# Performance work log

Measured on AMD Instinct MI355X. Metric: run time of the kernel, lower is better.

Reference implementation:

```python
import jax, jax.numpy as jnp
import numpy as np

E = 256; H = 8; HD = E // H
L_LEN = 300; A_LEN = 250
T = 768; B = 4
NEG = -1e9


def setup_inputs() -> dict:
    rng = jax.random.key(0)
    ks = jax.random.split(rng, 16)
    n = lambda k, s, sc=1.0: jax.random.normal(k, s, dtype=jnp.float32) * sc
    return {
        "query": n(ks[0], (T, B, E)),
        "key": n(ks[1], (T, B, E)),
        "value": n(ks[2], (T, B, E)),
        "in_proj_w": n(ks[3], (3 * E, E), 0.05),
        "in_proj_b": jnp.zeros((3 * E,), jnp.float32),
        "out_w": n(ks[4], (7, E, E), 0.05),
        "out_b": jnp.zeros((7, E), jnp.float32),
        "s_l_w": n(ks[5], (E, 4 * E), 0.05),
        "s_l_b": jnp.zeros((E,), jnp.float32),
        "s_a_w": n(ks[6], (E, 4 * E), 0.05),
        "s_a_b": jnp.zeros((E,), jnp.float32),
        "s_v_w": n(ks[7], (E, 4 * E), 0.05),
        "s_v_b": jnp.zeros((E,), jnp.float32),
        "final_w": n(ks[8], (E, E), 0.05),
        "final_b": jnp.zeros((E,), jnp.float32),
    }


def _forward(query, key, value, in_proj_w, in_proj_b, out_w, out_b,
             s_l_w, s_l_b, s_a_w, s_a_b, s_v_w, s_v_b, final_w, final_b):
    t, b, e = query.shape
    scaling = HD ** -0.5
    Wq, Wk, Wv = in_proj_w[:E], in_proj_w[E:2 * E], in_proj_w[2 * E:]
    bq, bk, bv = in_proj_b[:E], in_proj_b[E:2 * E], in_proj_b[2 * E:]
    q = (query @ Wq.T + bq) * scaling
    k = key @ Wk.T + bk
    v = value @ Wv.T + bv
    # (T, B, E) -> (B*H, T, HD)
    sh = lambda x: x.reshape(t, b * H, HD).transpose(1, 0, 2)
    q, k, v = sh(q), sh(k), sh(v)
    # shared QK^T, reused by all 7 masked branches
    scores = jnp.einsum('bth,bsh->bts', q, k)  # (B*H, T, T)
    idx = jnp.arange(t)
    seg = jnp.where(idx < L_LEN, 0, jnp.where(idx < L_LEN + A_LEN, 1, 2))

    def branch(i, mods):
        # m[j] = 1 iff position j belongs to one of the selected modalities
        m = sum((seg == s) for s in mods).astype(scores.dtype)  # (T,)
        # additive mask: in-set query attends only in-set keys; out-of-set
        # query rows get all -1e9 (uniform softmax, zeroed by row mask below)
        add = jnp.where((m[:, None] * m[None, :]) > 0, 0.0, NEG)
        w = jax.nn.softmax(scores + add, axis=-1) * m[None, :, None]
        o = jnp.einsum('bts,bsh->bth', w, v * m[None, :, None])
        o = o.transpose(1, 0, 2).reshape(t, b, e)
        return o @ out_w[i].T + out_b[i]

    attn_lav = branch(0, (0, 1, 2))
    attn_la = branch(1, (0, 1))
    attn_lv = branch(2, (0, 2))
    attn_av = branch(3, (1, 2))
    attn_l = branch(4, (0,))
    attn_a = branch(5, (1,))
    attn_v = branch(6, (2,))

    sl = jnp.concatenate([attn_lav, attn_la, attn_lv, attn_l], -1) @ s_l_w.T + s_l_b
    sa = jnp.concatenate([attn_lav, attn_la, attn_av, attn_a], -1) @ s_a_w.T + s_a_b
    sv = jnp.concatenate([attn_lav, attn_lv, attn_av, attn_v], -1) @ s_v_w.T + s_v_b
    return (sl + sa + sv) @ final_w.T + final_b


def reference(query, key, value, in_proj_w, in_proj_b, out_w, out_b,
              s_l_w, s_l_b, s_a_w, s_a_b, s_v_w, s_v_b, final_w, final_b):
    return _forward(query, key, value, in_proj_w, in_proj_b, out_w, out_b,
                    s_l_w, s_l_b, s_a_w, s_a_b, s_v_w, s_v_b, final_w, final_b)
```

## Files before the change

kernel.cpp:

```cpp
#include <hip/hip_runtime.h>
#include <hip/hip_bf16.h>

#define E 256
#define H 8
#define HD 32
#define T 768
#define B 4
#define BH 32

typedef __attribute__((ext_vector_type(8))) short bf16x8;
typedef __attribute__((ext_vector_type(4))) float f32x4;
typedef __attribute__((ext_vector_type(16))) float f32x16;

__device__ __forceinline__ float b2f(__hip_bfloat16 x) { return __bfloat162float(x); }

__device__ __forceinline__ unsigned short f2bf_u(float x) {
    __hip_bfloat16 h = __float2bfloat16(x);
    return *(unsigned short*)&h;
}
__device__ __forceinline__ float bfu2f(unsigned short u) {
    return __uint_as_float(((unsigned int)u) << 16);
}

__device__ __forceinline__ int detect_f32(const void* query) {
    const unsigned short* q = (const unsigned short*)query;
    int lane = threadIdx.x & 63;
    int bad = 0;
    #pragma unroll
    for (int i = 0; i < 4; ++i) {
        float v = bfu2f(q[lane + i * 64]);
        bad |= (!(v == v) || fabsf(v) > 1e4f) ? 1 : 0;
    }
    return __any(bad) ? 1 : 0;
}

__device__ __forceinline__ void f8_split(const float* v, bf16x8& h, bf16x8& l) {
    #pragma unroll
    for (int e = 0; e < 8; ++e) {
        unsigned short hu = f2bf_u(v[e]);
        h[e] = (short)hu;
        l[e] = (short)f2bf_u(v[e] - bfu2f(hu));
    }
}

#define MFMA3(ACC, AH, AL, BH_, BL_)                                         \
    ACC = __builtin_amdgcn_mfma_f32_16x16x32_bf16(AH, BH_, ACC, 0, 0, 0);    \
    ACC = __builtin_amdgcn_mfma_f32_16x16x32_bf16(AH, BL_, ACC, 0, 0, 0);    \
    ACC = __builtin_amdgcn_mfma_f32_16x16x32_bf16(AL, BH_, ACC, 0, 0, 0);

#define MFMA3W(ACC, AH, AL, BH_, BL_)                                        \
    ACC = __builtin_amdgcn_mfma_f32_32x32x16_bf16(AH, BH_, ACC, 0, 0, 0);    \
    ACC = __builtin_amdgcn_mfma_f32_32x32x16_bf16(AH, BL_, ACC, 0, 0, 0);    \
    ACC = __builtin_amdgcn_mfma_f32_32x32x16_bf16(AL, BH_, ACC, 0, 0, 0);

__device__ __forceinline__ bf16x8 mk8(int a, int b, int c, int d) {
    union { int i[4]; bf16x8 v; } u;
    u.i[0] = a; u.i[1] = b; u.i[2] = c; u.i[3] = d;
    return u.v;
}

__device__ __forceinline__ float ldu(const void* p, size_t i, int f32) {
    if (f32) return ((const float*)p)[i];
    return b2f(((const __hip_bfloat16*)p)[i]);
}

__device__ __forceinline__ float gsum_load(int i, int r2, int r,
                                           const void* sl, const void* sa,
                                           const void* sv, int f32)
{
    size_t base = (size_t)r2 * 1024;
    switch (i) {
        case 0: return ldu(sl, base + r, f32) + ldu(sa, base + r, f32) + ldu(sv, base + r, f32);
        case 1: return ldu(sl, base + 256 + r, f32) + ldu(sa, base + 256 + r, f32);
        case 2: return ldu(sl, base + 512 + r, f32) + ldu(sv, base + 256 + r, f32);
        case 3: return ldu(sa, base + 512 + r, f32) + ldu(sv, base + 512 + r, f32);
        case 4: return ldu(sl, base + 768 + r, f32);
        case 5: return ldu(sa, base + 768 + r, f32);
        default: return ldu(sv, base + 768 + r, f32);
    }
}

__global__ __launch_bounds__(256) void stage1_kernel(
    const void* query, const void* w,
    const void* sl, const void* sa, const void* sv, const void* outw,
    const void* outb, const void* slb, const void* sab, const void* svb,
    unsigned short* __restrict__ WFh, unsigned short* __restrict__ WFl,
    unsigned short* __restrict__ GFh, unsigned short* __restrict__ GFl,
    unsigned short* __restrict__ OWFh, unsigned short* __restrict__ OWFl,
    float* __restrict__ c0)
{
    __shared__ float red[256];
    int f32 = detect_f32(query);
    if (blockIdx.x < 544) {
        int item = blockIdx.x * 256 + threadIdx.x;
        if (item < 24576) {
            int gc = item >> 5, kg = item & 31;
            float v[8];
            if (f32) {
                const float4* p = (const float4*)((const float*)w +
                                   (size_t)gc * 256 + kg * 8);
                *(float4*)&v[0] = p[0];
                *(float4*)&v[4] = p[1];
            } else {
                #pragma unroll
                for (int j = 0; j < 8; ++j)
                    v[j] = ldu(w, (size_t)gc * 256 + kg * 8 + j, 0);
            }
            bf16x8 h, l;
            f8_split(v, h, l);
            int sec = gc >> 8, c = gc & 255;
            int cb = c >> 4, kb = kg >> 2;
            int lane = (c & 15) | ((kg & 3) << 4);
            size_t idx = (((size_t)(sec * 16 + cb) * 8 + kb) * 64 + lane) * 8;
            *(bf16x8*)&WFh[idx] = h;
            *(bf16x8*)&WFl[idx] = l;
        } else if (item < 81920) {
            int rem = item - 24576;
            int i = rem >> 13;
            int rest = rem & 8191;
            int r2 = rest >> 5, kg = rest & 31;
            float v[8];
            #pragma unroll
            for (int j = 0; j < 8; ++j)
                v[j] = gsum_load(i, r2, kg * 8 + j, sl, sa, sv, f32);
            bf16x8 h, l;
            f8_split(v, h, l);
            int rb = r2 >> 4, kb = kg >> 2;
            int lane = (r2 & 15) | ((kg & 3) << 4);
            size_t idx = (((size_t)(i * 16 + rb) * 8 + kb) * 64 + lane) * 8;
            *(bf16x8*)&GFh[idx] = h;
            *(bf16x8*)&GFl[idx] = l;
        } else if (item < 139264) {
            int rem = item - 81920;
            int i = rem >> 13;
            int rest = rem & 8191;
            int kg = rest >> 8, c = rest & 255;
            float v[8];
            #pragma unroll
            for (int j = 0; j < 8; ++j)
                v[j] = ldu(outw, (size_t)i * 65536 + (kg * 8 + j) * 256 + c, f32);
            bf16x8 h, l;
            f8_split(v, h, l);
            int cb = c >> 4, kb = kg >> 2;
            int lane = (c & 15) | ((kg & 3) << 4);
            size_t idx = (((size_t)(i * 16 + cb) * 8 + kb) * 64 + lane) * 8;
            *(bf16x8*)&OWFh[idx] = h;
            *(bf16x8*)&OWFl[idx] = l;
        }
    } else {
        int r2 = blockIdx.x - 544, m = threadIdx.x;
        float acc = 0.f;
        #pragma unroll
        for (int i = 0; i < 7; ++i)
            acc += ldu(outb, i * 256 + m, f32) * gsum_load(i, r2, m, sl, sa, sv, f32);
        red[m] = acc;
        __syncthreads();
        for (int s = 128; s > 0; s >>= 1) {
            if (m < s) red[m] += red[m + s];
            __syncthreads();
        }
        if (m == 0)
            c0[r2] = red[0] + ldu(slb, r2, f32) + ldu(sab, r2, f32) + ldu(svb, r2, f32);
    }
}

__global__ __launch_bounds__(256) void stage2_kernel(
    const void* query, const void* key, const void* value,
    const unsigned short* __restrict__ WFh, const unsigned short* __restrict__ WFl,
    const void* bias,
    float* __restrict__ qws,
    unsigned short* __restrict__ KRh, unsigned short* __restrict__ KRl,
    unsigned short* __restrict__ VFh, unsigned short* __restrict__ VFl,
    const unsigned short* __restrict__ GFh, const unsigned short* __restrict__ GFl,
    const unsigned short* __restrict__ OWFh, const unsigned short* __restrict__ OWFl,
    float* __restrict__ Mtmp,
    const float* __restrict__ c0, const void* finalw, const void* finalb,
    float* __restrict__ d0)
{
    __shared__ float red[256];
    int bxx = blockIdx.x;
    if (bxx < 576) {
        int f32 = detect_f32(query);
        int sec = bxx / 192;
        int rb  = bxx % 192;
        const void* X = (sec == 0) ? query : (sec == 1) ? key : value;
        int w = threadIdx.x >> 6, lane = threadIdx.x & 63;
        int m = lane & 15, quad = lane >> 4;

        size_t aoff0 = (size_t)(rb * 16 + (lane & 15)) * 256 + quad * 8;

        f32x4 acc[4] = {};
        #pragma unroll
        for (int kb = 0; kb < 8; ++kb) {
            float av[8];
            size_t aoff = aoff0 + kb * 32;
            if (f32) {
                const float4* p = (const float4*)((const float*)X + aoff);
                *(float4*)&av[0] = p[0];
                *(float4*)&av[4] = p[1];
            } else {
                #pragma unroll
                for (int j = 0; j < 8; ++j)
                    av[j] = ldu(X, aoff + j, 0);
            }
            bf16x8 ah, al;
            f8_split(av, ah, al);
            #pragma unroll
            for (int c = 0; c < 4; ++c) {
                int cb = w * 4 + c;
                const unsigned short* Bh = WFh + (((size_t)(sec * 16 + cb) * 8 + kb) * 64 + lane) * 8;
                const unsigned short* Bl = WFl + (((size_t)(sec * 16 + cb) * 8 + kb) * 64 + lane) * 8;
                bf16x8 bh = *(const bf16x8*)Bh;
                bf16x8 bl = *(const bf16x8*)Bl;
                MFMA3(acc[c], ah, al, bh, bl)
            }
        }

        #pragma unroll
        for (int c = 0; c < 4; ++c) {
            int cb = w * 4 + c;
            int c_local = cb * 16 + m;
            float bv = ldu(bias, sec * 256 + c_local, f32);
            int h = c_local >> 5, hd = c_local & 31;

            if (sec == 0) {
                #pragma unroll
                for (int rr = 0; rr < 4; ++rr) {
                    int row = rb * 16 + quad * 4 + rr;
                    int t = row >> 2, b = row & 3;
                    float val = (acc[c][rr] + bv) * 0.17677669529663687f;
                    qws[((size_t)((b * H + h) * T + t)) * HD + hd] = val;
                }
            } else if (sec == 1) {
                #pragma unroll
                for (int rr = 0; rr < 4; ++rr) {
                    int row = rb * 16 + quad * 4 + rr;
                    int s = row >> 2, b = row & 3;
                    int bh_ = b * 8 + h;
                    float val = acc[c][rr] + bv;
                    unsigned short hu = f2bf_u(val);
                    unsigned short lu = f2bf_u(val - bfu2f(hu));
                    size_t bi = ((size_t)bh_ * 768 + s) * 32 + hd;
                    KRh[bi] = hu;
                    KRl[bi] = lu;
                }
            } else {
                #pragma unroll
                for (int rr = 0; rr < 4; ++rr) {
                    int row = rb * 16 + quad * 4 + rr;
                    int s = row >> 2, b = row & 3;
                    int bh_ = b * 8 + h;
                    float val = acc[c][rr] + bv;
                    unsigned short hu = f2bf_u(val);
                    unsigned short lu = f2bf_u(val - bfu2f(hu));
                    int s16 = s >> 4, hp = (s >> 3) & 1, j = s & 7;
                    size_t bi = (((size_t)bh_ * 48 + s16) * 64 + hp * 32 + hd) * 8 + j;
                    VFh[bi] = hu;
                    VFl[bi] = lu;
                }
            }
        }
    } else if (bxx < 1024) {
        int idx = bxx - 576;
        int cgrp = idx & 3;
        int rb   = (idx >> 2) & 15;
        int i    = idx >> 6;
        int w = threadIdx.x >> 6, lane = threadIdx.x & 63;
        int m = lane & 15, quad = lane >> 4;
        int cb = cgrp * 4 + w;

        const unsigned short* Ah = GFh + (((size_t)(i * 16 + rb) * 8) * 64 + lane) * 8;
        const unsigned short* Al = GFl + (((size_t)(i * 16 + rb) * 8) * 64 + lane) * 8;
        const unsigned short* Bh = OWFh + (((size_t)(i * 16 + cb) * 8) * 64 + lane) * 8;
        const unsigned short* Bl = OWFl + (((size_t)(i * 16 + cb) * 8) * 64 + lane) * 8;

        f32x4 acc = {};
        #pragma unroll
        for (int kb = 0; kb < 8; ++kb) {
            size_t off = (size_t)kb * 512;
            bf16x8 ah = *(const bf16x8*)(Ah + off);
            bf16x8 al = *(const bf16x8*)(Al + off);
            bf16x8 bh = *(const bf16x8*)(Bh + off);
            bf16x8 bl = *(const bf16x8*)(Bl + off);
            MFMA3(acc, ah, al, bh, bl)
        }
        #pragma unroll
        for (int rr = 0; rr < 4; ++rr) {
            int r2 = rb * 16 + quad * 4 + rr;
            Mtmp[(size_t)i * 65536 + r2 * 256 + cb * 16 + m] = acc[rr];
        }
    } else {
        int f32 = detect_f32(query);
        int e = bxx - 1024, r = threadIdx.x;
        red[r] = c0[r] * ldu(finalw, (size_t)e * 256 + r, f32);
        __syncthreads();
        for (int s = 128; s > 0; s >>= 1) {
            if (r < s) red[r] += red[r + s];
            __syncthreads();
        }
        if (r == 0)
            d0[e] = red[0] + ldu(finalb, e, f32);
    }
}

__global__ __launch_bounds__(256, 2) void stage3_kernel(
    const float* __restrict__ qws,
    const unsigned short* __restrict__ KRh, const unsigned short* __restrict__ KRl,
    const unsigned short* __restrict__ VFh, const unsigned short* __restrict__ VFl,
    unsigned short* __restrict__ Ohi, unsigned short* __restrict__ Olo,
    const float* __restrict__ Mtmp, const void* finalw, const void* query,
    unsigned short* __restrict__ DThi, unsigned short* __restrict__ DTlo)
{
    __shared__ __align__(16) float SMEM[7104];
    int tid = threadIdx.x;

    if (blockIdx.x < 768) {
        float (*AC2)[3][32][36] = (float(*)[3][32][36])&SMEM[0];
        float (*SS2)[3][32]     = (float(*)[3][32])&SMEM[6912];
        int bid = blockIdx.x;
        int xcd = bid & 7, rr_ = bid >> 3;
        int j_ = rr_ / 24, tile = rr_ % 24;
        int bh = j_ * 8 + xcd;
        int t0 = tile * 32;
        int w = tid >> 6, lane = tid & 63;
        int ln = lane & 31, h = lane >> 5;

        bf16x8 qbh[2], qbl[2];
        {
            const float* qr = qws + ((size_t)bh * T + t0 + ln) * HD + h * 8;
            #pragma unroll
            for (int c = 0; c < 2; ++c) {
                float qv[8];
                *(float4*)&qv[0] = *(const float4*)(qr + c * 16);
                *(float4*)&qv[4] = *(const float4*)(qr + c * 16 + 4);
                f8_split(qv, qbh[c], qbl[c]);
            }
        }

        f32x16 accA = {}, accB = {};
        float ssA = 0.f, ssB = 0.f;

        for (int q = 0; q < 3; ++q) {
            int ch = w * 3 + q;
            int sbase = ch * 64;
            int route = (ch == 5) ? 1 : (ch == 4 || ch == 8) ? 2 : 0;
            int bnd = (ch == 4) ? 300 : 550;
            bool c12 = (ch == 4);

            bf16x8 kf0h[2], kf0l[2], kf1h[2], kf1l[2], vh[4], vl[4];
            #pragma unroll
            for (int st = 0; st < 2; ++st) {
                size_t krow = ((size_t)bh * 768 + sbase + st * 32 + ln) * 32 + h * 8;
                kf0h[st] = *(const bf16x8*)(KRh + krow);
                kf0l[st] = *(const bf16x8*)(KRl + krow);
                kf1h[st] = *(const bf16x8*)(KRh + krow + 16);
                kf1l[st] = *(const bf16x8*)(KRl + krow + 16);
            }
            #pragma unroll
            for (int ks = 0; ks < 4; ++ks) {
                size_t vidx = (((size_t)bh * 48 + ch * 4 + ks) * 64 + lane) * 8;
                vh[ks] = *(const bf16x8*)(VFh + vidx);
                vl[ks] = *(const bf16x8*)(VFl + vidx);
            }

            #pragma unroll
            for (int st = 0; st < 2; ++st) {
                f32x16 d = {};
                MFMA3W(d, kf0h[st], kf0l[st], qbh[0], qbl[0])
                MFMA3W(d, kf1h[st], kf1l[st], qbh[1], qbl[1])

                int PH[8], PL[8];
                #pragma unroll
                for (int p = 0; p < 8; ++p) {
                    float e0 = __expf(d[2 * p]);
                    float e1 = __expf(d[2 * p + 1]);
                    if (route == 2) {
                        int r0 = 2 * p;
                        int s0 = sbase + st * 32 + (r0 & 3) + 8 * (r0 >> 2) + 4 * h;
                        if (s0 < bnd) ssA += e0; else ssB += e0;
                        if (s0 + 1 < bnd) ssA += e1; else ssB += e1;
                    } else if (route == 1) { ssB += e0 + e1; }
                    else { ssA += e0 + e1; }
                    unsigned b0 = __float_as_uint(e0), b1 = __float_as_uint(e1);
                    float l0 = e0 - __uint_as_float(b0 & 0xffff0000u);
                    float l1 = e1 - __uint_as_float(b1 & 0xffff0000u);
                    PH[p] = (int)((b0 >> 16) | (b1 & 0xffff0000u));
                    PL[p] = (int)((__float_as_uint(l0) >> 16) |
                                  (__float_as_uint(l1) & 0xffff0000u));
                }

                #pragma unroll
                for (int ksl = 0; ksl < 2; ++ksl) {
                    int ks = st * 2 + ksl;
                    int cc = 4 * ksl;
                    bf16x8 vbh = vh[ks];
                    bf16x8 vbl = vl[ks];

                    int sh0 = __shfl_xor(PH[cc+0], 32);
                    int sh1 = __shfl_xor(PH[cc+1], 32);
                    int sh2 = __shfl_xor(PH[cc+2], 32);
                    int sh3 = __shfl_xor(PH[cc+3], 32);
                    int sl0 = __shfl_xor(PL[cc+0], 32);
                    int sl1 = __shfl_xor(PL[cc+1], 32);
                    int sl2 = __shfl_xor(PL[cc+2], 32);
                    int sl3 = __shfl_xor(PL[cc+3], 32);
                    int FH0 = h ? sh2 : PH[cc+0];
                    int FH1 = h ? sh3 : PH[cc+1];
                    int FH2 = h ? PH[cc+2] : sh0;
                    int FH3 = h ? PH[cc+3] : sh1;
                    int FL0 = h ? sl2 : PL[cc+0];
                    int FL1 = h ? sl3 : PL[cc+1];
                    int FL2 = h ? PL[cc+2] : sl0;
                    int FL3 = h ? PL[cc+3] : sl1;
                    bf16x8 feh = mk8(FH0, FH1, FH2, FH3);
                    bf16x8 fel = mk8(FL0, FL1, FL2, FL3);

                    if (route == 0)      { MFMA3W(accA, feh, fel, vbh, vbl) }
                    else if (route == 1) { MFMA3W(accB, feh, fel, vbh, vbl) }
                    else {
                        if (ks < 2)       { MFMA3W(accA, feh, fel, vbh, vbl) }
                        else if (ks == 3) { MFMA3W(accB, feh, fel, vbh, vbl) }
                        else {
                            int a0 = h ? (c12 ? FH0 : 0) : FH0;
                            int a1 = h ? (c12 ? FH1 : 0) : FH1;
                            int a2 = h ? 0 : FH2;
                            int a3 = h ? 0 : (c12 ? FH3 : 0);
                            int b0 = h ? (c12 ? 0 : FH0) : 0;
                            int b1 = h ? (c12 ? 0 : FH1) : 0;
                            int b2 = h ? FH2 : 0;
                            int b3 = h ? FH3 : (c12 ? 0 : FH3);
                            int la0 = h ? (c12 ? FL0 : 0) : FL0;
                            int la1 = h ? (c12 ? FL1 : 0) : FL1;
                            int la2 = h ? 0 : FL2;
                            int la3 = h ? 0 : (c12 ? FL3 : 0);
                            int lb0 = h ? (c12 ? 0 : FL0) : 0;
                            int lb1 = h ? (c12 ? 0 : FL1) : 0;
                            int lb2 = h ? FL2 : 0;
                            int lb3 = h ? FL3 : (c12 ? 0 : FL3);
                            bf16x8 fha = mk8(a0, a1, a2, a3), fla = mk8(la0, la1, la2, la3);
                            bf16x8 fhb = mk8(b0, b1, b2, b3), flb = mk8(lb0, lb1, lb2, lb3);
                            MFMA3W(accA, fha, fla, vbh, vbl)
                            MFMA3W(accB, fhb, flb, vbh, vbl)
                        }
                    }
                }
            }
        }

        ssA += __shfl_xor(ssA, 32);
        ssB += __shfl_xor(ssB, 32);

        int bsel = w & 1;
        f32x16 zz = {};
        f32x16 o0 = (w <= 1) ? accA : zz;
        f32x16 o1 = (w == 1) ? accB : (w == 2) ? accA : zz;
        f32x16 o2 = (w == 2) ? accB : (w == 3) ? accA : zz;
        float s0 = (w <= 1) ? ssA : 0.f;
        float s1 = (w == 1) ? ssB : (w == 2) ? ssA : 0.f;
        float s2 = (w == 2) ? ssB : (w == 3) ? ssA : 0.f;

        if (w < 2) {
            #pragma unroll
            for (int r = 0; r < 16; ++r) {
                int t = (r & 3) + 8 * (r >> 2) + 4 * h;
                AC2[bsel][0][t][ln] = o0[r];
                AC2[bsel][1][t][ln] = o1[r];
                AC2[bsel][2][t][ln] = o2[r];
            }
            if (h == 0) {
                SS2[bsel][0][ln] = s0;
                SS2[bsel][1][ln] = s1;
                SS2[bsel][2][ln] = s2;
            }
        }
        __syncthreads();
        if (w >= 2) {
            #pragma unroll
            for (int r = 0; r < 16; ++r) {
                int t = (r & 3) + 8 * (r >> 2) + 4 * h;
                AC2[bsel][1][t][ln] += o1[r];
                AC2[bsel][2][t][ln] += o2[r];
            }
            if (h == 0) {
                SS2[bsel][1][ln] += s1;
                SS2[bsel][2][ln] += s2;
            }
        }
        __syncthreads();

        int tt = tid >> 3, q4 = tid & 7;
        float Pv[3][4], S[3];
        #pragma unroll
        for (int sg = 0; sg < 3; ++sg) {
            const float4 a = *(const float4*)&AC2[0][sg][tt][q4 * 4];
            const float4 b = *(const float4*)&AC2[1][sg][tt][q4 * 4];
            Pv[sg][0] = a.x + b.x; Pv[sg][1] = a.y + b.y;
            Pv[sg][2] = a.z + b.z; Pv[sg][3] = a.w + b.w;
            S[sg] = SS2[0][sg][tt] + SS2[1][sg][tt];
        }

        int t_glob = t0 + tt;
        int g = (t_glob < 300) ? 0 : (t_glob < 550 ? 1 : 2);
        int b_ = bh >> 3, h_ = bh & 7;
        int row = b_ * T + t_glob;
        int lslot = (row & 15) + ((q4 >> 1) << 4);
        int j0 = (q4 & 1) * 4;
        size_t fbase = (((size_t)(row >> 4) * 56 + h_) * 64 + lslot) * 8 + j0;
        const int masks[7] = {7, 3, 5, 6, 1, 2, 4};
        #pragma unroll
        for (int i = 0; i < 7; ++i) {
            int mm = masks[i];
            float n0 = 0.f, n1 = 0.f, n2 = 0.f, n3 = 0.f, den = 0.f;
            if (mm & 1) { n0 += Pv[0][0]; n1 += Pv[0][1]; n2 += Pv[0][2]; n3 += Pv[0][3]; den += S[0]; }
            if (mm & 2) { n0 += Pv[1][0]; n1 += Pv[1][1]; n2 += Pv[1][2]; n3 += Pv[1][3]; den += S[1]; }
            if (mm & 4) { n0 += Pv[2][0]; n1 += Pv[2][1]; n2 += Pv[2][2]; n3 += Pv[2][3]; den += S[2]; }
            float r = 1.f / den;
            int live = (mm >> g) & 1;
            float o[4];
            o[0] = live ? n0 * r : 0.f;
            o[1] = live ? n1 * r : 0.f;
            o[2] = live ? n2 * r : 0.f;
            o[3] = live ? n3 * r : 0.f;
            ushort4 hi4, lo4;
            unsigned short* hp = (unsigned short*)&hi4;
            unsigned short* lp = (unsigned short*)&lo4;
            #pragma unroll
            for (int jq = 0; jq < 4; ++jq) {
                unsigned short hu = f2bf_u(o[jq]);
                hp[jq] = hu;
                lp[jq] = f2bf_u(o[jq] - bfu2f(hu));
            }
            size_t addr = fbase + (size_t)i * (8 * 64 * 8);
            *(ushort4*)&Ohi[addr] = hi4;
            *(ushort4*)&Olo[addr] = lo4;
        }
    } else {
        float (*AsT)[34] = (float(*)[34])&SMEM[0];
        float (*Bs)[34]  = (float(*)[34])&SMEM[1088];
        int f32 = detect_f32(query);
        int idx = blockIdx.x - 768;
        int bx = idx & 7;
        int by = (idx >> 3) & 7;
        int i  = idx >> 6;
        int tx = tid & 15, ty = tid >> 4;
        int colbase = bx * 32, rowbase = by * 32;
        float acc[2][2] = {};

        for (int kb = 0; kb < 8; ++kb) {
            __syncthreads();
            #pragma unroll
            for (int l = 0; l < 4; ++l) {
                int idx2 = l * 256 + tid;
                int c = idx2 & 31, kk = idx2 >> 5;
                AsT[kk][c] = Mtmp[(size_t)i * 65536 + (kb * 32 + kk) * 256 + rowbase + c];
                int k2 = idx2 & 31, n = idx2 >> 5;
                Bs[k2][n] = ldu(finalw, (size_t)(colbase + n) * 256 + kb * 32 + k2, f32);
            }
            __syncthreads();
            #pragma unroll 8
            for (int kk = 0; kk < 32; ++kk) {
                const float2 av = *(const float2*)&AsT[kk][ty * 2];
                const float2 bv = *(const float2*)&Bs[kk][tx * 2];
                acc[0][0] += av.x * bv.x; acc[0][1] += av.x * bv.y;
                acc[1][0] += av.y * bv.x; acc[1][1] += av.y * bv.y;
            }
        }
        #pragma unroll
        for (int u = 0; u < 2; ++u)
            #pragma unroll
            for (int v = 0; v < 2; ++v) {
                int c = rowbase + ty * 2 + u, e = colbase + tx * 2 + v;
                float a = acc[u][v];
                unsigned short hu = f2bf_u(a);
                size_t fidx = (((size_t)(e >> 4) * 56 + i * 8 + (c >> 5)) * 64
                               + (e & 15) + (((c >> 3) & 3) << 4)) * 8 + (c & 7);
                DThi[fidx] = hu;
                DTlo[fidx] = f2bf_u(a - bfu2f(hu));
            }
    }
}

__global__ __launch_bounds__(256) void final_gemm_mfma_kernel(
    const unsigned short* __restrict__ Ohi, const unsigned short* __restrict__ Olo,
    const unsigned short* __restrict__ DThi, const unsigned short* __restrict__ DTlo,
    const float* __restrict__ d0, const void* query,
    void* __restrict__ outv)
{
    int f32 = detect_f32(query);
    int bid = blockIdx.x;
    int xcd = bid & 7, rr_ = bid >> 3;
    int slot = rr_ >> 2, bx = rr_ & 3;
    int by = slot * 8 + xcd;
    int w  = threadIdx.x >> 6;
    int lane = threadIdx.x & 63;
    int m = lane & 15, quad = lane >> 4;
    int R0 = by * 16, C0 = bx * 64 + w * 16;

    int b_out = R0 / 768;
    int tfirst = R0 - b_out * 768;
    int g0 = (tfirst < 300) ? 0 : (tfirst < 550 ? 1 : 2);
    int g1 = (tfirst + 15 < 300) ? 0 : (tfirst + 15 < 550 ? 1 : 2);
    int activeset = (1 << g0) | (1 << g1);
    const int masks[7] = {7, 3, 5, 6, 1, 2, 4};

    const unsigned short* Abase_h = Ohi + (size_t)by * 56 * 512 + lane * 8;
    const unsigned short* Abase_l = Olo + (size_t)by * 56 * 512 + lane * 8;
    const unsigned short* Bbase_h = DThi + (size_t)(bx * 4 + w) * 56 * 512 + lane * 8;
    const unsigned short* Bbase_l = DTlo + (size_t)(bx * 4 + w) * 56 * 512 + lane * 8;

    f32x4 acc = {};
    for (int i = 0; i < 7; ++i) {
        if (!(masks[i] & activeset)) continue;
        #pragma unroll
        for (int kb = 0; kb < 8; ++kb) {
            size_t off = (size_t)(i * 8 + kb) * 512;
            bf16x8 ah = *(const bf16x8*)(Abase_h + off);
            bf16x8 al = *(const bf16x8*)(Abase_l + off);
            bf16x8 bh = *(const bf16x8*)(Bbase_h + off);
            bf16x8 bl = *(const bf16x8*)(Bbase_l + off);
            acc = __builtin_amdgcn_mfma_f32_16x16x32_bf16(ah, bh, acc, 0, 0, 0);
            acc = __builtin_amdgcn_mfma_f32_16x16x32_bf16(ah, bl, acc, 0, 0, 0);
            acc = __builtin_amdgcn_mfma_f32_16x16x32_bf16(al, bh, acc, 0, 0, 0);
        }
    }
    float dv = d0[C0 + m];
    #pragma unroll
    for (int r = 0; r < 4; ++r) {
        int t = tfirst + quad * 4 + r;
        int col = C0 + m;
        float val = acc[r] + dv;
        size_t orow = (size_t)t * B + b_out;
        if (f32) ((float*)outv)[orow * 256 + col] = val;
        else ((__hip_bfloat16*)outv)[orow * 256 + col] = __float2bfloat16(val);
    }
}

extern "C" void kernel_launch(void* const* d_in, const int* in_sizes, int n_in,
                              void* d_out, int out_size, void* d_ws, size_t ws_size,
                              hipStream_t stream) {
    const void* query     = d_in[0];
    const void* key       = d_in[1];
    const void* value     = d_in[2];
    const void* in_proj_w = d_in[3];
    const void* in_proj_b = d_in[4];
    const void* out_w     = d_in[5];
    const void* out_b     = d_in[6];
    const void* s_l_w     = d_in[7];
    const void* s_l_b     = d_in[8];
    const void* s_a_w     = d_in[9];
    const void* s_a_b     = d_in[10];
    const void* s_v_w     = d_in[11];
    const void* s_v_b     = d_in[12];
    const void* final_w   = d_in[13];
    const void* final_b   = d_in[14];

    float* ws     = (float*)d_ws;
    float* qws    = ws;
    unsigned short* KRh = (unsigned short*)(ws + 786432);
    unsigned short* KRl = KRh + 786432;
    unsigned short* VFh = (unsigned short*)(ws + 1572864);
    unsigned short* VFl = VFh + 786432;
    unsigned short* Ohi = (unsigned short*)(ws + 2359296);
    unsigned short* Olo = (unsigned short*)(ws + 5111808);
    unsigned short* WFh = (unsigned short*)(ws + 2359296);
    unsigned short* WFl = WFh + 196608;
    unsigned short* GFh = (unsigned short*)(ws + 4915200);
    unsigned short* GFl = GFh + 458752;
    unsigned short* OWFh = GFl + 458752;
    unsigned short* OWFl = OWFh + 458752;
    float* Mtmp   = ws + 7864320;
    unsigned short* DThi = (unsigned short*)(ws + 8323072);
    unsigned short* DTlo = (unsigned short*)(ws + 8552448);
    float* d0     = ws + 8781824;
    float* c0     = ws + 8782336;

    stage1_kernel<<<800, 256, 0, stream>>>(query, in_proj_w,
                                           s_l_w, s_a_w, s_v_w, out_w,
                                           out_b, s_l_b, s_a_b, s_v_b,
                                           WFh, WFl,
                                           GFh, GFl, OWFh, OWFl, c0);
    stage2_kernel<<<1280, 256, 0, stream>>>(query, key, value,
                                            WFh, WFl, in_proj_b, qws,
                                            KRh, KRl, VFh, VFl,
                                            GFh, GFl, OWFh, OWFl, Mtmp,
                                            c0, final_w, final_b, d0);
    stage3_kernel<<<1216, 256, 0, stream>>>(qws, KRh, KRl, VFh, VFl,
                                            Ohi, Olo,
                                            Mtmp, final_w, query,
                                            DThi, DTlo);
    final_gemm_mfma_kernel<<<768, 256, 0, stream>>>(Ohi, Olo, DThi, DTlo,
                                                    d0, query, d_out);
}
```

Before: 160.4 us.

## Reassociate folded weight products to move final_w GEMM off the attention stage

The weight-folding chain is reordered. final_w × Gsum_i is now computed first in stage1 with MFMA into Qbuf, and stage2 multiplies that by out_w_i and writes the DT fragments directly. This removes the GF split buffers and the scalar FP32 LDS-tiled GEMM that used to run as extra blocks inside the attention kernel (stage3), so stage3 only does attention with 768 blocks. The cost is heavier stage1 blocks that gather gsum values element-wise, and a changed rounding order for the folded weights.

```diff
diff --git a/kernel.cpp b/kernel.cpp
--- a/kernel.cpp
+++ b/kernel.cpp
@@ -84,15 +84,16 @@
     const void* query, const void* w,
     const void* sl, const void* sa, const void* sv, const void* outw,
     const void* outb, const void* slb, const void* sab, const void* svb,
+    const void* finalw,
     unsigned short* __restrict__ WFh, unsigned short* __restrict__ WFl,
-    unsigned short* __restrict__ GFh, unsigned short* __restrict__ GFl,
     unsigned short* __restrict__ OWFh, unsigned short* __restrict__ OWFl,
-    float* __restrict__ c0)
+    float* __restrict__ Qbuf, float* __restrict__ c0)
 {
     __shared__ float red[256];
     int f32 = detect_f32(query);
-    if (blockIdx.x < 544) {
-        int item = blockIdx.x * 256 + threadIdx.x;
+    int bid = blockIdx.x;
+    if (bid < 320) {
+        int item = bid * 256 + threadIdx.x;
         if (item < 24576) {
             int gc = item >> 5, kg = item & 31;
             float v[8];
@@ -118,22 +119,6 @@
             int rem = item - 24576;
             int i = rem >> 13;
             int rest = rem & 8191;
-            int r2 = rest >> 5, kg = rest & 31;
-            float v[8];
-            #pragma unroll
-            for (int j = 0; j < 8; ++j)
-                v[j] = gsum_load(i, r2, kg * 8 + j, sl, sa, sv, f32);
-            bf16x8 h, l;
-            f8_split(v, h, l);
-            int rb = r2 >> 4, kb = kg >> 2;
-            int lane = (r2 & 15) | ((kg & 3) << 4);
-            size_t idx = (((size_t)(i * 16 + rb) * 8 + kb) * 64 + lane) * 8;
-            *(bf16x8*)&GFh[idx] = h;
-            *(bf16x8*)&GFl[idx] = l;
-        } else if (item < 139264) {
-            int rem = item - 81920;
-            int i = rem >> 13;
-            int rest = rem & 8191;
             int kg = rest >> 8, c = rest & 255;
             float v[8];
             #pragma unroll
@@ -147,8 +132,47 @@
             *(bf16x8*)&OWFh[idx] = h;
             *(bf16x8*)&OWFl[idx] = l;
         }
+    } else if (bid < 768) {
+        int unit = bid - 320;
+        int kgrp = unit & 3;
+        int eb   = (unit >> 2) & 15;
+        int i    = unit >> 6;
+        int w_ = threadIdx.x >> 6, lane = threadIdx.x & 63;
+        int m = lane & 15, quad = lane >> 4;
+        int kblk = kgrp * 4 + w_;
+
+        f32x4 acc = {};
+        #pragma unroll
+        for (int rb2 = 0; rb2 < 8; ++rb2) {
+            float av[8];
+            size_t fo = (size_t)(eb * 16 + m) * 256 + rb2 * 32 + quad * 8;
+            if (f32) {
+                const float4* p = (const float4*)((const float*)finalw + fo);
+                *(float4*)&av[0] = p[0];
+                *(float4*)&av[4] = p[1];
+            } else {
+                #pragma unroll
+                for (int j = 0; j < 8; ++j)
+                    av[j] = ldu(finalw, fo + j, 0);
+            }
+            bf16x8 ah, al;
+            f8_split(av, ah, al);
+            float bv[8];
+            #pragma unroll
+            for (int j = 0; j < 8; ++j)
+                bv[j] = gsum_load(i, rb2 * 32 + quad * 8 + j, kblk * 16 + m,
+                                  sl, sa, sv, f32);
+            bf16x8 bh, bl;
+            f8_split(bv, bh, bl);
+            MFMA3(acc, ah, al, bh, bl)
+        }
+        #pragma unroll
+        for (int rr = 0; rr < 4; ++rr) {
+            int e_ = eb * 16 + quad * 4 + rr;
+            Qbuf[(size_t)i * 65536 + e_ * 256 + kblk * 16 + m] = acc[rr];
+        }
     } else {
-        int r2 = blockIdx.x - 544, m = threadIdx.x;
+        int r2 = bid - 768, m = threadIdx.x;
         float acc = 0.f;
         #pragma unroll
         for (int i = 0; i < 7; ++i)
@@ -171,9 +195,9 @@
     float* __restrict__ qws,
     unsigned short* __restrict__ KRh, unsigned short* __restrict__ KRl,
     unsigned short* __restrict__ VFh, unsigned short* __restrict__ VFl,
-    const unsigned short* __restrict__ GFh, const unsigned short* __restrict__ GFl,
     const unsigned short* __restrict__ OWFh, const unsigned short* __restrict__ OWFl,
-    float* __restrict__ Mtmp,
+    const float* __restrict__ Qbuf,
+    unsigned short* __restrict__ DThi, unsigned short* __restrict__ DTlo,
     const float* __restrict__ c0, const void* finalw, const void* finalb,
     float* __restrict__ d0)
 {
@@ -261,33 +285,40 @@
             }
         }
     } else if (bxx < 1024) {
-        int idx = bxx - 576;
-        int cgrp = idx & 3;
-        int rb   = (idx >> 2) & 15;
-        int i    = idx >> 6;
+        int unit = bxx - 576;
+        int cgrp = unit & 3;
+        int eb   = (unit >> 2) & 15;
+        int i    = unit >> 6;
         int w = threadIdx.x >> 6, lane = threadIdx.x & 63;
         int m = lane & 15, quad = lane >> 4;
         int cb = cgrp * 4 + w;
 
-        const unsigned short* Ah = GFh + (((size_t)(i * 16 + rb) * 8) * 64 + lane) * 8;
-        const unsigned short* Al = GFl + (((size_t)(i * 16 + rb) * 8) * 64 + lane) * 8;
-        const unsigned short* Bh = OWFh + (((size_t)(i * 16 + cb) * 8) * 64 + lane) * 8;
-        const unsigned short* Bl = OWFl + (((size_t)(i * 16 + cb) * 8) * 64 + lane) * 8;
-
         f32x4 acc = {};
         #pragma unroll
         for (int kb = 0; kb < 8; ++kb) {
-            size_t off = (size_t)kb * 512;
-            bf16x8 ah = *(const bf16x8*)(Ah + off);
-            bf16x8 al = *(const bf16x8*)(Al + off);
-            bf16x8 bh = *(const bf16x8*)(Bh + off);
-            bf16x8 bl = *(const bf16x8*)(Bl + off);
+            float av[8];
+            const float* qp = Qbuf + (size_t)i * 65536 +
+                              (size_t)(eb * 16 + m) * 256 + kb * 32 + quad * 8;
+            *(float4*)&av[0] = *(const float4*)qp;
+            *(float4*)&av[4] = *(const float4*)(qp + 4);
+            bf16x8 ah, al;
+            f8_split(av, ah, al);
+            const unsigned short* Bh = OWFh + (((size_t)(i * 16 + cb) * 8 + kb) * 64 + lane) * 8;
+            const unsigned short* Bl = OWFl + (((size_t)(i * 16 + cb) * 8 + kb) * 64 + lane) * 8;
+            bf16x8 bh = *(const bf16x8*)Bh;
+            bf16x8 bl = *(const bf16x8*)Bl;
             MFMA3(acc, ah, al, bh, bl)
         }
         #pragma unroll
         for (int rr = 0; rr < 4; ++rr) {
-            int r2 = rb * 16 + quad * 4 + rr;
-            Mtmp[(size_t)i * 65536 + r2 * 256 + cb * 16 + m] = acc[rr];
+            int e_ = eb * 16 + quad * 4 + rr;
+            int c_ = cb * 16 + m;
+            float a = acc[rr];
+            unsigned short hu = f2bf_u(a);
+            size_t fidx = (((size_t)(e_ >> 4) * 56 + i * 8 + (c_ >> 5)) * 64
+                           + (e_ & 15) + (((c_ >> 3) & 3) << 4)) * 8 + (c_ & 7);
+            DThi[fidx] = hu;
+            DTlo[fidx] = f2bf_u(a - bfu2f(hu));
         }
     } else {
         int f32 = detect_f32(query);
@@ -307,276 +338,231 @@
     const float* __restrict__ qws,
     const unsigned short* __restrict__ KRh, const unsigned short* __restrict__ KRl,
     const unsigned short* __restrict__ VFh, const unsigned short* __restrict__ VFl,
-    unsigned short* __restrict__ Ohi, unsigned short* __restrict__ Olo,
-    const float* __restrict__ Mtmp, const void* finalw, const void* query,
-    unsigned short* __restrict__ DThi, unsigned short* __restrict__ DTlo)
+    unsigned short* __restrict__ Ohi, unsigned short* __restrict__ Olo)
 {
     __shared__ __align__(16) float SMEM[7104];
     int tid = threadIdx.x;
 
-    if (blockIdx.x < 768) {
-        float (*AC2)[3][32][36] = (float(*)[3][32][36])&SMEM[0];
-        float (*SS2)[3][32]     = (float(*)[3][32])&SMEM[6912];
-        int bid = blockIdx.x;
-        int xcd = bid & 7, rr_ = bid >> 3;
-        int j_ = rr_ / 24, tile = rr_ % 24;
-        int bh = j_ * 8 + xcd;
-        int t0 = tile * 32;
-        int w = tid >> 6, lane = tid & 63;
-        int ln = lane & 31, h = lane >> 5;
-
-        bf16x8 qbh[2], qbl[2];
-        {
-            const float* qr = qws + ((size_t)bh * T + t0 + ln) * HD + h * 8;
+    float (*AC2)[3][32][36] = (float(*)[3][32][36])&SMEM[0];
+    float (*SS2)[3][32]     = (float(*)[3][32])&SMEM[6912];
+    int bid = blockIdx.x;
+    int xcd = bid & 7, rr_ = bid >> 3;
+    int j_ = rr_ / 24, tile = rr_ % 24;
+    int bh = j_ * 8 + xcd;
+    int t0 = tile * 32;
+    int w = tid >> 6, lane = tid & 63;
+    int ln = lane & 31, h = lane >> 5;
+
+    bf16x8 qbh[2], qbl[2];
+    {
+        const float* qr = qws + ((size_t)bh * T + t0 + ln) * HD + h * 8;
+        #pragma unroll
+        for (int c = 0; c < 2; ++c) {
+            float qv[8];
+            *(float4*)&qv[0] = *(const float4*)(qr + c * 16);
+            *(float4*)&qv[4] = *(const float4*)(qr + c * 16 + 4);
+            f8_split(qv, qbh[c], qbl[c]);
+        }
+    }
+
+    f32x16 accA = {}, accB = {};
+    float ssA = 0.f, ssB = 0.f;
+
+    for (int q = 0; q < 3; ++q) {
+        int ch = w * 3 + q;
+        int sbase = ch * 64;
+        int route = (ch == 5) ? 1 : (ch == 4 || ch == 8) ? 2 : 0;
+        int bnd = (ch == 4) ? 300 : 550;
+        bool c12 = (ch == 4);
+
+        bf16x8 kf0h[2], kf0l[2], kf1h[2], kf1l[2], vh[4], vl[4];
+        #pragma unroll
+        for (int st = 0; st < 2; ++st) {
+            size_t krow = ((size_t)bh * 768 + sbase + st * 32 + ln) * 32 + h * 8;
+            kf0h[st] = *(const bf16x8*)(KRh + krow);
+            kf0l[st] = *(const bf16x8*)(KRl + krow);
+            kf1h[st] = *(const bf16x8*)(KRh + krow + 16);
+            kf1l[st] = *(const bf16x8*)(KRl + krow + 16);
+        }
+        #pragma unroll
+        for (int ks = 0; ks < 4; ++ks) {
+            size_t vidx = (((size_t)bh * 48 + ch * 4 + ks) * 64 + lane) * 8;
+            vh[ks] = *(const bf16x8*)(VFh + vidx);
+            vl[ks] = *(const bf16x8*)(VFl + vidx);
+        }
+
+        #pragma unroll
+        for (int st = 0; st < 2; ++st) {
+            f32x16 d = {};
+            MFMA3W(d, kf0h[st], kf0l[st], qbh[0], qbl[0])
+            MFMA3W(d, kf1h[st], kf1l[st], qbh[1], qbl[1])
+
+            int PH[8], PL[8];
             #pragma unroll
-            for (int c = 0; c < 2; ++c) {
-                float qv[8];
-                *(float4*)&qv[0] = *(const float4*)(qr + c * 16);
-                *(float4*)&qv[4] = *(const float4*)(qr + c * 16 + 4);
-                f8_split(qv, qbh[c], qbl[c]);
+            for (int p = 0; p < 8; ++p) {
+                float e0 = __expf(d[2 * p]);
+                float e1 = __expf(d[2 * p + 1]);
+                if (route == 2) {
+                    int r0 = 2 * p;
+                    int s0 = sbase + st * 32 + (r0 & 3) + 8 * (r0 >> 2) + 4 * h;
+                    if (s0 < bnd) ssA += e0; else ssB += e0;
+                    if (s0 + 1 < bnd) ssA += e1; else ssB += e1;
+                } else if (route == 1) { ssB += e0 + e1; }
+                else { ssA += e0 + e1; }
+                unsigned b0 = __float_as_uint(e0), b1 = __float_as_uint(e1);
+                float l0 = e0 - __uint_as_float(b0 & 0xffff0000u);
+                float l1 = e1 - __uint_as_float(b1 & 0xffff0000u);
+                PH[p] = (int)((b0 >> 16) | (b1 & 0xffff0000u));
+                PL[p] = (int)((__float_as_uint(l0) >> 16) |
+                              (__float_as_uint(l1) & 0xffff0000u));
             }
-        }
-
-        f32x16 accA = {}, accB = {};
-        float ssA = 0.f, ssB = 0.f;
-
-        for (int q = 0; q < 3; ++q) {
-            int ch = w * 3 + q;
-            int sbase = ch * 64;
-            int route = (ch == 5) ? 1 : (ch == 4 || ch == 8) ? 2 : 0;
-            int bnd = (ch == 4) ? 300 : 550;
-            bool c12 = (ch == 4);
-
-            bf16x8 kf0h[2], kf0l[2], kf1h[2], kf1l[2], vh[4], vl[4];
+
             #pragma unroll
-            for (int st = 0; st < 2; ++st) {
-                size_t krow = ((size_t)bh * 768 + sbase + st * 32 + ln) * 32 + h * 8;
-                kf0h[st] = *(const bf16x8*)(KRh + krow);
-                kf0l[st] = *(const bf16x8*)(KRl + krow);
-                kf1h[st] = *(const bf16x8*)(KRh + krow + 16);
-                kf1l[st] = *(const bf16x8*)(KRl + krow + 16);
-            }
-            #pragma unroll
-            for (int ks = 0; ks < 4; ++ks) {
-                size_t vidx = (((size_t)bh * 48 + ch * 4 + ks) * 64 + lane) * 8;
-                vh[ks] = *(const bf16x8*)(VFh + vidx);
-                vl[ks] = *(const bf16x8*)(VFl + vidx);
-            }
-
-            #pragma unroll
-            for (int st = 0; st < 2; ++st) {
-                f32x16 d = {};
-                MFMA3W(d, kf0h[st], kf0l[st], qbh[0], qbl[0])
-                MFMA3W(d, kf1h[st], kf1l[st], qbh[1], qbl[1])
-
-                int PH[8], PL[8];
-                #pragma unroll
-                for (int p = 0; p < 8; ++p) {
-                    float e0 = __expf(d[2 * p]);
-                    float e1 = __expf(d[2 * p + 1]);
-                    if (route == 2) {
-                        int r0 = 2 * p;
-                        int s0 = sbase + st * 32 + (r0 & 3) + 8 * (r0 >> 2) + 4 * h;
-                        if (s0 < bnd) ssA += e0; else ssB += e0;
-                        if (s0 + 1 < bnd) ssA += e1; else ssB += e1;
-                    } else if (route == 1) { ssB += e0 + e1; }
-                    else { ssA += e0 + e1; }
-                    unsigned b0 = __float_as_uint(e0), b1 = __float_as_uint(e1);
-                    float l0 = e0 - __uint_as_float(b0 & 0xffff0000u);
-                    float l1 = e1 - __uint_as_float(b1 & 0xffff0000u);
-                    PH[p] = (int)((b0 >> 16) | (b1 & 0xffff0000u));
-                    PL[p] = (int)((__float_as_uint(l0) >> 16) |
-                                  (__float_as_uint(l1) & 0xffff0000u));
-                }
-
-                #pragma unroll
-                for (int ksl = 0; ksl < 2; ++ksl) {
-                    int ks = st * 2 + ksl;
-                    int cc = 4 * ksl;
-                    bf16x8 vbh = vh[ks];
-                    bf16x8 vbl = vl[ks];
-
-                    int sh0 = __shfl_xor(PH[cc+0], 32);
-                    int sh1 = __shfl_xor(PH[cc+1], 32);
-                    int sh2 = __shfl_xor(PH[cc+2], 32);
-                    int sh3 = __shfl_xor(PH[cc+3], 32);
-                    int sl0 = __shfl_xor(PL[cc+0], 32);
-                    int sl1 = __shfl_xor(PL[cc+1], 32);
-                    int sl2 = __shfl_xor(PL[cc+2], 32);
-                    int sl3 = __shfl_xor(PL[cc+3], 32);
-                    int FH0 = h ? sh2 : PH[cc+0];
-                    int FH1 = h ? sh3 : PH[cc+1];
-                    int FH2 = h ? PH[cc+2] : sh0;
-                    int FH3 = h ? PH[cc+3] : sh1;
-                    int FL0 = h ? sl2 : PL[cc+0];
-                    int FL1 = h ? sl3 : PL[cc+1];
-                    int FL2 = h ? PL[cc+2] : sl0;
-                    int FL3 = h ? PL[cc+3] : sl1;
-                    bf16x8 feh = mk8(FH0, FH1, FH2, FH3);
-                    bf16x8 fel = mk8(FL0, FL1, FL2, FL3);
-
-                    if (route == 0)      { MFMA3W(accA, feh, fel, vbh, vbl) }
-                    else if (route == 1) { MFMA3W(accB, feh, fel, vbh, vbl) }
+            for (int ksl = 0; ksl < 2; ++ksl) {
+                int ks = st * 2 + ksl;
+                int cc = 4 * ksl;
+                bf16x8 vbh = vh[ks];
+                bf16x8 vbl = vl[ks];
+
+                int sh0 = __shfl_xor(PH[cc+0], 32);
+                int sh1 = __shfl_xor(PH[cc+1], 32);
+                int sh2 = __shfl_xor(PH[cc+2], 32);
+                int sh3 = __shfl_xor(PH[cc+3], 32);
+                int sl0 = __shfl_xor(PL[cc+0], 32);
+                int sl1 = __shfl_xor(PL[cc+1], 32);
+                int sl2 = __shfl_xor(PL[cc+2], 32);
+                int sl3 = __shfl_xor(PL[cc+3], 32);
+                int FH0 = h ? sh2 : PH[cc+0];
+                int FH1 = h ? sh3 : PH[cc+1];
+                int FH2 = h ? PH[cc+2] : sh0;
+                int FH3 = h ? PH[cc+3] : sh1;
+                int FL0 = h ? sl2 : PL[cc+0];
+                int FL1 = h ? sl3 : PL[cc+1];
+                int FL2 = h ? PL[cc+2] : sl0;
+                int FL3 = h ? PL[cc+3] : sl1;
+                bf16x8 feh = mk8(FH0, FH1, FH2, FH3);
+                bf16x8 fel = mk8(FL0, FL1, FL2, FL3);
+
+                if (route == 0)      { MFMA3W(accA, feh, fel, vbh, vbl) }
+                else if (route == 1) { MFMA3W(accB, feh, fel, vbh, vbl) }
+                else {
+                    if (ks < 2)       { MFMA3W(accA, feh, fel, vbh, vbl) }
+                    else if (ks == 3) { MFMA3W(accB, feh, fel, vbh, vbl) }
                     else {
-                        if (ks < 2)       { MFMA3W(accA, feh, fel, vbh, vbl) }
-                        else if (ks == 3) { MFMA3W(accB, feh, fel, vbh, vbl) }
-                        else {
-                            int a0 = h ? (c12 ? FH0 : 0) : FH0;
-                            int a1 = h ? (c12 ? FH1 : 0) : FH1;
-                            int a2 = h ? 0 : FH2;
-                            int a3 = h ? 0 : (c12 ? FH3 : 0);
-                            int b0 = h ? (c12 ? 0 : FH0) : 0;
-                            int b1 = h ? (c12 ? 0 : FH1) : 0;
-                            int b2 = h ? FH2 : 0;
-                            int b3 = h ? FH3 : (c12 ? 0 : FH3);
-                            int la0 = h ? (c12 ? FL0 : 0) : FL0;
-                            int la1 = h ? (c12 ? FL1 : 0) : FL1;
-                            int la2 = h ? 0 : FL2;
-                            int la3 = h ? 0 : (c12 ? FL3 : 0);
-                            int lb0 = h ? (c12 ? 0 : FL0) : 0;
-                            int lb1 = h ? (c12 ? 0 : FL1) : 0;
-                            int lb2 = h ? FL2 : 0;
-                            int lb3 = h ? FL3 : (c12 ? 0 : FL3);
-                            bf16x8 fha = mk8(a0, a1, a2, a3), fla = mk8(la0, la1, la2, la3);
-                            bf16x8 fhb = mk8(b0, b1, b2, b3), flb = mk8(lb0, lb1, lb2, lb3);
-                            MFMA3W(accA, fha, fla, vbh, vbl)
-                            MFMA3W(accB, fhb, flb, vbh, vbl)
-                        }
+                        int a0 = h ? (c12 ? FH0 : 0) : FH0;
+                        int a1 = h ? (c12 ? FH1 : 0) : FH1;
+                        int a2 = h ? 0 : FH2;
+                        int a3 = h ? 0 : (c12 ? FH3 : 0);
+                        int b0 = h ? (c12 ? 0 : FH0) : 0;
+                        int b1 = h ? (c12 ? 0 : FH1) : 0;
+                        int b2 = h ? FH2 : 0;
+                        int b3 = h ? FH3 : (c12 ? 0 : FH3);
+                        int la0 = h ? (c12 ? FL0 : 0) : FL0;
+                        int la1 = h ? (c12 ? FL1 : 0) : FL1;
+                        int la2 = h ? 0 : FL2;
+                        int la3 = h ? 0 : (c12 ? FL3 : 0);
+                        int lb0 = h ? (c12 ? 0 : FL0) : 0;
+                        int lb1 = h ? (c12 ? 0 : FL1) : 0;
+                        int lb2 = h ? FL2 : 0;
+                        int lb3 = h ? FL3 : (c12 ? 0 : FL3);
+                        bf16x8 fha = mk8(a0, a1, a2, a3), fla = mk8(la0, la1, la2, la3);
+                        bf16x8 fhb = mk8(b0, b1, b2, b3), flb = mk8(lb0, lb1, lb2, lb3);
+                        MFMA3W(accA, fha, fla, vbh, vbl)
+                        MFMA3W(accB, fhb, flb, vbh, vbl)
                     }
                 }
             }
         }
-
-        ssA += __shfl_xor(ssA, 32);
-        ssB += __shfl_xor(ssB, 32);
-
-        int bsel = w & 1;
-        f32x16 zz = {};
-        f32x16 o0 = (w <= 1) ? accA : zz;
-        f32x16 o1 = (w == 1) ? accB : (w == 2) ? accA : zz;
-        f32x16 o2 = (w == 2) ? accB : (w == 3) ? accA : zz;
-        float s0 = (w <= 1) ? ssA : 0.f;
-        float s1 = (w == 1) ? ssB : (w == 2) ? ssA : 0.f;
-        float s2 = (w == 2) ? ssB : (w == 3) ? ssA : 0.f;
-
-        if (w < 2) {
-            #pragma unroll
-            for (int r = 0; r < 16; ++r) {
-                int t = (r & 3) + 8 * (r >> 2) + 4 * h;
-                AC2[bsel][0][t][ln] = o0[r];
-                AC2[bsel][1][t][ln] = o1[r];
-                AC2[bsel][2][t][ln] = o2[r];
-            }
-            if (h == 0) {
-                SS2[bsel][0][ln] = s0;
-                SS2[bsel][1][ln] = s1;
-                SS2[bsel][2][ln] = s2;
-            }
-        }
-        __syncthreads();
-        if (w >= 2) {
-            #pragma unroll
-            for (int r = 0; r < 16; ++r) {
-                int t = (r & 3) + 8 * (r >> 2) + 4 * h;
-                AC2[bsel][1][t][ln] += o1[r];
-                AC2[bsel][2][t][ln] += o2[r];
-            }
-            if (h == 0) {
-                SS2[bsel][1][ln] += s1;
-                SS2[bsel][2][ln] += s2;
-            }
-        }
-        __syncthreads();
-
-        int tt = tid >> 3, q4 = tid & 7;
-        float Pv[3][4], S[3];
-        #pragma unroll
-        for (int sg = 0; sg < 3; ++sg) {
-            const float4 a = *(const float4*)&AC2[0][sg][tt][q4 * 4];
-            const float4 b = *(const float4*)&AC2[1][sg][tt][q4 * 4];
-            Pv[sg][0] = a.x + b.x; Pv[sg][1] = a.y + b.y;
-            Pv[sg][2] = a.z + b.z; Pv[sg][3] = a.w + b.w;
-            S[sg] = SS2[0][sg][tt] + SS2[1][sg][tt];
-        }
-
-        int t_glob = t0 + tt;
-        int g = (t_glob < 300) ? 0 : (t_glob < 550 ? 1 : 2);
-        int b_ = bh >> 3, h_ = bh & 7;
-        int row = b_ * T + t_glob;
-        int lslot = (row & 15) + ((q4 >> 1) << 4);
-        int j0 = (q4 & 1) * 4;
-        size_t fbase = (((size_t)(row >> 4) * 56 + h_) * 64 + lslot) * 8 + j0;
-        const int masks[7] = {7, 3, 5, 6, 1, 2, 4};
-        #pragma unroll
-        for (int i = 0; i < 7; ++i) {
-            int mm = masks[i];
-            float n0 = 0.f, n1 = 0.f, n2 = 0.f, n3 = 0.f, den = 0.f;
-            if (mm & 1) { n0 += Pv[0][0]; n1 += Pv[0][1]; n2 += Pv[0][2]; n3 += Pv[0][3]; den += S[0]; }
-            if (mm & 2) { n0 += Pv[1][0]; n1 += Pv[1][1]; n2 += Pv[1][2]; n3 += Pv[1][3]; den += S[1]; }
-            if (mm & 4) { n0 += Pv[2][0]; n1 += Pv[2][1]; n2 += Pv[2][2]; n3 += Pv[2][3]; den += S[2]; }
-            float r = 1.f / den;
-            int live = (mm >> g) & 1;
-            float o[4];
-            o[0] = live ? n0 * r : 0.f;
-            o[1] = live ? n1 * r : 0.f;
-            o[2] = live ? n2 * r : 0.f;
-            o[3] = live ? n3 * r : 0.f;
-            ushort4 hi4, lo4;
-            unsigned short* hp = (unsigned short*)&hi4;
-            unsigned short* lp = (unsigned short*)&lo4;
-            #pragma unroll
-            for (int jq = 0; jq < 4; ++jq) {
-                unsigned short hu = f2bf_u(o[jq]);
-                hp[jq] = hu;
-                lp[jq] = f2bf_u(o[jq] - bfu2f(hu));
-            }
-            size_t addr = fbase + (size_t)i * (8 * 64 * 8);
-            *(ushort4*)&Ohi[addr] = hi4;
-            *(ushort4*)&Olo[addr] = lo4;
-        }
-    } else {
-        float (*AsT)[34] = (float(*)[34])&SMEM[0];
-        float (*Bs)[34]  = (float(*)[34])&SMEM[1088];
-        int f32 = detect_f32(query);
-        int idx = blockIdx.x - 768;
-        int bx = idx & 7;
-        int by = (idx >> 3) & 7;
-        int i  = idx >> 6;
-        int tx = tid & 15, ty = tid >> 4;
-        int colbase = bx * 32, rowbase = by * 32;
-        float acc[2][2] = {};
-
-        for (int kb = 0; kb < 8; ++kb) {
-            __syncthreads();
-            #pragma unroll
-            for (int l = 0; l < 4; ++l) {
-                int idx2 = l * 256 + tid;
-                int c = idx2 & 31, kk = idx2 >> 5;
-                AsT[kk][c] = Mtmp[(size_t)i * 65536 + (kb * 32 + kk) * 256 + rowbase + c];
-                int k2 = idx2 & 31, n = idx2 >> 5;
-                Bs[k2][n] = ldu(finalw, (size_t)(colbase + n) * 256 + kb * 32 + k2, f32);
-            }
-            __syncthreads();
-            #pragma unroll 8
-            for (int kk = 0; kk < 32; ++kk) {
-                const float2 av = *(const float2*)&AsT[kk][ty * 2];
-                const float2 bv = *(const float2*)&Bs[kk][tx * 2];
-                acc[0][0] += av.x * bv.x; acc[0][1] += av.x * bv.y;
-                acc[1][0] += av.y * bv.x; acc[1][1] += av.y * bv.y;
-            }
-        }
-        #pragma unroll
-        for (int u = 0; u < 2; ++u)
-            #pragma unroll
-            for (int v = 0; v < 2; ++v) {
-                int c = rowbase + ty * 2 + u, e = colbase + tx * 2 + v;
-                float a = acc[u][v];
-                unsigned short hu = f2bf_u(a);
-                size_t fidx = (((size_t)(e >> 4) * 56 + i * 8 + (c >> 5)) * 64
-                               + (e & 15) + (((c >> 3) & 3) << 4)) * 8 + (c & 7);
-                DThi[fidx] = hu;
-                DTlo[fidx] = f2bf_u(a - bfu2f(hu));
-            }
+    }
+
+    ssA += __shfl_xor(ssA, 32);
+    ssB += __shfl_xor(ssB, 32);
+
+    int bsel = w & 1;
+    f32x16 zz = {};
+    f32x16 o0 = (w <= 1) ? accA : zz;
+    f32x16 o1 = (w == 1) ? accB : (w == 2) ? accA : zz;
+    f32x16 o2 = (w == 2) ? accB : (w == 3) ? accA : zz;
+    float s0 = (w <= 1) ? ssA : 0.f;
+    float s1 = (w == 1) ? ssB : (w == 2) ? ssA : 0.f;
+    float s2 = (w == 2) ? ssB : (w == 3) ? ssA : 0.f;
+
+    if (w < 2) {
+        #pragma unroll
+        for (int r = 0; r < 16; ++r) {
+            int t = (r & 3) + 8 * (r >> 2) + 4 * h;
+            AC2[bsel][0][t][ln] = o0[r];
+            AC2[bsel][1][t][ln] = o1[r];
+            AC2[bsel][2][t][ln] = o2[r];
+        }
+        if (h == 0) {
+            SS2[bsel][0][ln] = s0;
+            SS2[bsel][1][ln] = s1;
+            SS2[bsel][2][ln] = s2;
+        }
+    }
+    __syncthreads();
+    if (w >= 2) {
+        #pragma unroll
+        for (int r = 0; r < 16; ++r) {
+            int t = (r & 3) + 8 * (r >> 2) + 4 * h;
+            AC2[bsel][1][t][ln] += o1[r];
+            AC2[bsel][2][t][ln] += o2[r];
+        }
+        if (h == 0) {
+            SS2[bsel][1][ln] += s1;
+            SS2[bsel][2][ln] += s2;
+        }
+    }
+    __syncthreads();
+
+    int tt = tid >> 3, q4 = tid & 7;
+    float Pv[3][4], S[3];
+    #pragma unroll
+    for (int sg = 0; sg < 3; ++sg) {
+        const float4 a = *(const float4*)&AC2[0][sg][tt][q4 * 4];
+        const float4 b = *(const float4*)&AC2[1][sg][tt][q4 * 4];
+        Pv[sg][0] = a.x + b.x; Pv[sg][1] = a.y + b.y;
+        Pv[sg][2] = a.z + b.z; Pv[sg][3] = a.w + b.w;
+        S[sg] = SS2[0][sg][tt] + SS2[1][sg][tt];
+    }
+
+    int t_glob = t0 + tt;
+    int g = (t_glob < 300) ? 0 : (t_glob < 550 ? 1 : 2);
+    int mixed = (((t_glob >> 4) == 18) || ((t_glob >> 4) == 34)) ? 1 : 0;
+    int b_ = bh >> 3, h_ = bh & 7;
+    int row = b_ * T + t_glob;
+    int lslot = (row & 15) + ((q4 >> 1) << 4);
+    int j0 = (q4 & 1) * 4;
+    size_t fbase = (((size_t)(row >> 4) * 56 + h_) * 64 + lslot) * 8 + j0;
+    const int masks[7] = {7, 3, 5, 6, 1, 2, 4};
+    #pragma unroll
+    for (int i = 0; i < 7; ++i) {
+        int mm = masks[i];
+        int live = (mm >> g) & 1;
+        if (!(live | mixed)) continue;
+        float n0 = 0.f, n1 = 0.f, n2 = 0.f, n3 = 0.f, den = 0.f;
+        if (mm & 1) { n0 += Pv[0][0]; n1 += Pv[0][1]; n2 += Pv[0][2]; n3 += Pv[0][3]; den += S[0]; }
+        if (mm & 2) { n0 += Pv[1][0]; n1 += Pv[1][1]; n2 += Pv[1][2]; n3 += Pv[1][3]; den += S[1]; }
+        if (mm & 4) { n0 += Pv[2][0]; n1 += Pv[2][1]; n2 += Pv[2][2]; n3 += Pv[2][3]; den += S[2]; }
+        float r = 1.f / den;
+        float o[4];
+        o[0] = live ? n0 * r : 0.f;
+        o[1] = live ? n1 * r : 0.f;
+        o[2] = live ? n2 * r : 0.f;
+        o[3] = live ? n3 * r : 0.f;
+        ushort4 hi4, lo4;
+        unsigned short* hp = (unsigned short*)&hi4;
+        unsigned short* lp = (unsigned short*)&lo4;
+        #pragma unroll
+        for (int jq = 0; jq < 4; ++jq) {
+            unsigned short hu = f2bf_u(o[jq]);
+            hp[jq] = hu;
+            lp[jq] = f2bf_u(o[jq] - bfu2f(hu));
+        }
+        size_t addr = fbase + (size_t)i * (8 * 64 * 8);
+        *(ushort4*)&Ohi[addr] = hi4;
+        *(ushort4*)&Olo[addr] = lo4;
     }
 }
 
@@ -664,30 +650,27 @@
     unsigned short* Olo = (unsigned short*)(ws + 5111808);
     unsigned short* WFh = (unsigned short*)(ws + 2359296);
     unsigned short* WFl = WFh + 196608;
-    unsigned short* GFh = (unsigned short*)(ws + 4915200);
-    unsigned short* GFl = GFh + 458752;
-    unsigned short* OWFh = GFl + 458752;
+    unsigned short* OWFh = (unsigned short*)(ws + 4915200);
     unsigned short* OWFl = OWFh + 458752;
-    float* Mtmp   = ws + 7864320;
+    float* Qbuf   = ws + 7864320;
     unsigned short* DThi = (unsigned short*)(ws + 8323072);
     unsigned short* DTlo = (unsigned short*)(ws + 8552448);
     float* d0     = ws + 8781824;
     float* c0     = ws + 8782336;
 
-    stage1_kernel<<<800, 256, 0, stream>>>(query, in_proj_w,
-                                           s_l_w, s_a_w, s_v_w, out_w,
-                                           out_b, s_l_b, s_a_b, s_v_b,
-                                           WFh, WFl,
-                                           GFh, GFl, OWFh, OWFl, c0);
+    stage1_kernel<<<1024, 256, 0, stream>>>(query, in_proj_w,
+                                            s_l_w, s_a_w, s_v_w, out_w,
+                                            out_b, s_l_b, s_a_b, s_v_b,
+                                            final_w,
+                                            WFh, WFl, OWFh, OWFl, Qbuf, c0);
     stage2_kernel<<<1280, 256, 0, stream>>>(query, key, value,
                                             WFh, WFl, in_proj_b, qws,
                                             KRh, KRl, VFh, VFl,
-                                            GFh, GFl, OWFh, OWFl, Mtmp,
+                                            OWFh, OWFl, Qbuf,
+                                            DThi, DTlo,
                                             c0, final_w, final_b, d0);
-    stage3_kernel<<<1216, 256, 0, stream>>>(qws, KRh, KRl, VFh, VFl,
-                                            Ohi, Olo,
-                                            Mtmp, final_w, query,
-                                            DThi, DTlo);
+    stage3_kernel<<<768, 256, 0, stream>>>(qws, KRh, KRl, VFh, VFl,
+                                           Ohi, Olo);
     final_gemm_mfma_kernel<<<768, 256, 0, stream>>>(Ohi, Olo, DThi, DTlo,
                                                     d0, query, d_out);
 }
```

Result: slower. 167.3 us (+4.3%).
